# Optimization experiments

Hardware: AMD Instinct MI355X
Metric: run time of the kernel (lower is better)

## Reference

```python
import jax, jax.numpy as jnp
import numpy as np

B, N, QD = 1, 4096, 1024
H, DH = 16, 64  # heads, dim_head; inner_dim = H*DH = 1024
SCALE = DH ** -0.5


def setup_inputs() -> dict:
    key = jax.random.key(0)
    ks = jax.random.split(key, 6)
    inner = H * DH
    return {
        "x": jax.random.normal(ks[0], (B, N, QD), dtype=jnp.float32),
        "Wq": jax.random.normal(ks[1], (QD, inner), dtype=jnp.float32) * (QD ** -0.5),
        "Wk": jax.random.normal(ks[2], (QD, inner), dtype=jnp.float32) * (QD ** -0.5),
        "Wv": jax.random.normal(ks[3], (QD, inner), dtype=jnp.float32) * (QD ** -0.5),
        "Wo": jax.random.normal(ks[4], (inner, QD), dtype=jnp.float32) * (inner ** -0.5),
        "bo": jnp.zeros((QD,), dtype=jnp.float32),
    }


def reference(x, Wq, Wk, Wv, Wo, bo):
    b, n, _ = x.shape
    # projections, split heads: b n (h d) -> b h n d
    q = (x @ Wq).reshape(b, n, H, DH).transpose(0, 2, 1, 3)
    k = (x @ Wk).reshape(b, n, H, DH).transpose(0, 2, 1, 3)
    v = (x @ Wv).reshape(b, n, H, DH).transpose(0, 2, 1, 3)
    # fp32-forced QK^T (ATTN_PRECISION='fp32' path), then scale
    sim = jnp.einsum("bhid,bhjd->bhij", q.astype(jnp.float32), k.astype(jnp.float32)) * SCALE
    attn = jax.nn.softmax(sim, axis=-1)
    out = jnp.einsum("bhij,bhjd->bhid", attn, v)  # b h n d
    out = out.transpose(0, 2, 1, 3).reshape(b, n, H * DH)  # merge heads
    return out @ Wo + bo
```

## Files before the change

### kernel.cpp

```cpp
#include <hip/hip_runtime.h>
#include <stdint.h>

#define NH 16
#define NN 4096

typedef __attribute__((ext_vector_type(8))) short bf16x8;
typedef __attribute__((ext_vector_type(4))) short bf16x4;
typedef __attribute__((ext_vector_type(4))) float f32x4;
typedef __attribute__((ext_vector_type(16))) float f32x16;
typedef unsigned short u16;
typedef unsigned int u32;
typedef __attribute__((ext_vector_type(4))) u32 u32x4;

__device__ __forceinline__ u16 f2bf(float f) {
  u32 u = __float_as_uint(f);
  return (u16)((u + 0x7FFFu + ((u >> 16) & 1u)) >> 16);
}

#define GLD16(gp, lp)                                              \
  __builtin_amdgcn_global_load_lds(                                \
      (__attribute__((address_space(1))) void*)(gp),               \
      (__attribute__((address_space(3))) void*)(lp), 16, 0, 0)

__global__ __launch_bounds__(256) void cvt_bf16_kernel(const float* __restrict__ src,
                                                       u16* __restrict__ dst, int n) {
  int i = (blockIdx.x * blockDim.x + threadIdx.x) * 8;
  if (i >= n) return;
  float4 a = *(const float4*)(src + i);
  float4 b = *(const float4*)(src + i + 4);
  uint4 o;
  o.x = (u32)f2bf(a.x) | ((u32)f2bf(a.y) << 16);
  o.y = (u32)f2bf(a.z) | ((u32)f2bf(a.w) << 16);
  o.z = (u32)f2bf(b.x) | ((u32)f2bf(b.y) << 16);
  o.w = (u32)f2bf(b.z) | ((u32)f2bf(b.w) << 16);
  *(uint4*)(dst + i) = o;
}

__global__ __launch_bounds__(256) void transpose4(const float* __restrict__ Wq,
                                                  const float* __restrict__ Wk,
                                                  const float* __restrict__ Wv,
                                                  const float* __restrict__ Wo,
                                                  u16* __restrict__ Wqt, u16* __restrict__ Wkt,
                                                  u16* __restrict__ Wvt, u16* __restrict__ Wot) {
  __shared__ float tile[64][65];
  const float* src;
  u16* dst;
  float scale = 1.0f;
  int z = blockIdx.z;
  if (z == 0) { src = Wq; dst = Wqt; scale = 0.125f * 1.4426950408889634f; }
  else if (z == 1) { src = Wk; dst = Wkt; }
  else if (z == 2) { src = Wv; dst = Wvt; }
  else { src = Wo; dst = Wot; }
  int tx = threadIdx.x & 63, ty = threadIdx.x >> 6;
  int c0 = blockIdx.x * 64, r0 = blockIdx.y * 64;
#pragma unroll
  for (int i = ty; i < 64; i += 4)
    tile[i][tx] = src[(size_t)(r0 + i) * 1024 + c0 + tx];
  __syncthreads();
#pragma unroll
  for (int i = ty; i < 64; i += 4)
    dst[(size_t)(c0 + i) * 1024 + r0 + tx] = f2bf(tile[tx][i] * scale);
}

__global__ __launch_bounds__(256) void gemm_qkv(const u16* __restrict__ A,
                                                const u16* __restrict__ Bt,
                                                u16* __restrict__ Qb, u16* __restrict__ Kb,
                                                u16* __restrict__ Vth) {
  __shared__ __align__(16) u16 A_lds[2][128 * 32];
  __shared__ __align__(16) u16 B_lds[2][128 * 32];
  const int tid = threadIdx.x;
  const int l = tid & 63, w = tid >> 6;
  const int g = l >> 4, c = l & 15;
  const int wr = w >> 1, wc = w & 1;
  const int m0 = blockIdx.y * 128, n0 = blockIdx.x * 128;

  const int srow = tid >> 2;
  const u32 sswz = (u32)(((tid & 3) * 16) ^ ((srow & 3) << 4));
  const char* Ag = (const char*)A + (size_t)(m0 + srow) * 2048 + sswz;
  const char* Bg = (const char*)Bt + (size_t)(n0 + srow) * 2048 + sswz;
  const u32 ldsb = (u32)(w * 1024);

#define GSTAGE(buf, ks_)                                                          \
  do {                                                                            \
    u32 koff_ = (u32)(ks_) * 64;                                                  \
    _Pragma("unroll") for (int p_ = 0; p_ < 2; ++p_) {                            \
      GLD16(Ag + koff_ + (size_t)p_ * 64 * 2048,                                  \
            (char*)A_lds[buf] + p_ * 4096 + ldsb);                                \
      GLD16(Bg + koff_ + (size_t)p_ * 64 * 2048,                                  \
            (char*)B_lds[buf] + p_ * 4096 + ldsb);                                \
    }                                                                             \
  } while (0)

  f32x4 acc[4][4];
#pragma unroll
  for (int i = 0; i < 4; ++i)
#pragma unroll
    for (int j = 0; j < 4; ++j) acc[i][j] = (f32x4){0.f, 0.f, 0.f, 0.f};

  int cur = 0;
  GSTAGE(0, 0);
  for (int ks = 0; ks < 32; ++ks) {
    GSTAGE(cur ^ 1, (ks + 1) & 31);
    asm volatile("s_waitcnt vmcnt(4)" ::: "memory");
    __builtin_amdgcn_s_barrier();
    __builtin_amdgcn_sched_barrier(0);
    const char* Ac = (const char*)A_lds[cur];
    const char* Bc = (const char*)B_lds[cur];
    bf16x8 af[4], bfr[4];
#pragma unroll
    for (int i = 0; i < 4; ++i) {
      int row = wr * 64 + i * 16 + c;
      af[i] = *(const bf16x8*)(Ac + row * 64 + ((g * 16) ^ ((row & 3) << 4)));
    }
#pragma unroll
    for (int j = 0; j < 4; ++j) {
      int row = wc * 64 + j * 16 + c;
      bfr[j] = *(const bf16x8*)(Bc + row * 64 + ((g * 16) ^ ((row & 3) << 4)));
    }
    __builtin_amdgcn_s_setprio(1);
#pragma unroll
    for (int i = 0; i < 4; ++i)
#pragma unroll
      for (int j = 0; j < 4; ++j)
        acc[i][j] = __builtin_amdgcn_mfma_f32_16x16x32_bf16(af[i], bfr[j], acc[i][j], 0, 0, 0);
    __builtin_amdgcn_s_setprio(0);
    asm volatile("s_waitcnt lgkmcnt(0)" ::: "memory");
    __builtin_amdgcn_s_barrier();
    __builtin_amdgcn_sched_barrier(0);
    cur ^= 1;
  }
#undef GSTAGE

  const int sec = n0 >> 10;
  const int gq = ((g & 1) << 1) | (g >> 1);
#pragma unroll
  for (int i = 0; i < 4; ++i)
#pragma unroll
    for (int j = 0; j < 4; ++j)
#pragma unroll
      for (int r = 0; r < 4; ++r) {
        int m = m0 + wr * 64 + i * 16 + g * 4 + r;
        int col = n0 + wc * 64 + j * 16 + c;
        int cc = col & 1023;
        u16 v = f2bf(acc[i][j][r]);
        if (sec == 0) Qb[(size_t)m * 1024 + cc] = v;
        else if (sec == 1) Kb[(size_t)m * 1024 + cc] = v;
        else {
          int mq = m0 + wr * 64 + i * 16 + gq * 4 + r;
          Vth[(size_t)cc * 4096 + mq] = v;
        }
      }
}

__global__ __launch_bounds__(256) void gemm_out128(const u16* __restrict__ A,
                                                   const u16* __restrict__ Bt,
                                                   float* __restrict__ out,
                                                   const float* __restrict__ bias) {
  __shared__ __align__(16) u16 A_lds[2][128 * 32];
  __shared__ __align__(16) u16 B_lds[2][64 * 32];
  const int tid = threadIdx.x;
  const int l = tid & 63, w = tid >> 6;
  const int g = l >> 4, c = l & 15;
  const int m0 = blockIdx.y * 128, n0 = blockIdx.x * 64;

  const int srow = tid >> 2;
  const u32 sswz = (u32)(((tid & 3) * 16) ^ ((srow & 3) << 4));
  const char* Ag = (const char*)A + (size_t)(m0 + srow) * 2048 + sswz;
  const char* Bg = (const char*)Bt + (size_t)(n0 + srow) * 2048 + sswz;
  const u32 ldsb = (u32)(w * 1024);

#define GSTAGE3(buf, ks_)                                                         \
  do {                                                                            \
    u32 koff_ = (u32)(ks_) * 64;                                                  \
    GLD16(Ag + koff_, (char*)A_lds[buf] + ldsb);                                  \
    GLD16(Ag + koff_ + (size_t)64 * 2048, (char*)A_lds[buf] + 4096 + ldsb);       \
    GLD16(Bg + koff_, (char*)B_lds[buf] + ldsb);                                  \
  } while (0)

  f32x4 acc[2][4];
#pragma unroll
  for (int i = 0; i < 2; ++i)
#pragma unroll
    for (int j = 0; j < 4; ++j) acc[i][j] = (f32x4){0.f, 0.f, 0.f, 0.f};

  int cur = 0;
  GSTAGE3(0, 0);
  for (int ks = 0; ks < 32; ++ks) {
    GSTAGE3(cur ^ 1, (ks + 1) & 31);
    asm volatile("s_waitcnt vmcnt(3)" ::: "memory");
    __builtin_amdgcn_s_barrier();
    __builtin_amdgcn_sched_barrier(0);
    const char* Ac = (const char*)A_lds[cur];
    const char* Bc = (const char*)B_lds[cur];
    bf16x8 af[2], bfr[4];
#pragma unroll
    for (int i = 0; i < 2; ++i) {
      int row = w * 32 + i * 16 + c;
      af[i] = *(const bf16x8*)(Ac + row * 64 + ((g * 16) ^ ((row & 3) << 4)));
    }
#pragma unroll
    for (int j = 0; j < 4; ++j) {
      int row = j * 16 + c;
      bfr[j] = *(const bf16x8*)(Bc + row * 64 + ((g * 16) ^ ((row & 3) << 4)));
    }
    __builtin_amdgcn_s_setprio(1);
#pragma unroll
    for (int i = 0; i < 2; ++i)
#pragma unroll
      for (int j = 0; j < 4; ++j)
        acc[i][j] = __builtin_amdgcn_mfma_f32_16x16x32_bf16(af[i], bfr[j], acc[i][j], 0, 0, 0);
    __builtin_amdgcn_s_setprio(0);
    asm volatile("s_waitcnt lgkmcnt(0)" ::: "memory");
    __builtin_amdgcn_s_barrier();
    __builtin_amdgcn_sched_barrier(0);
    cur ^= 1;
  }
#undef GSTAGE3

#pragma unroll
  for (int i = 0; i < 2; ++i)
#pragma unroll
    for (int j = 0; j < 4; ++j)
#pragma unroll
      for (int r = 0; r < 4; ++r) {
        int m = m0 + w * 32 + i * 16 + g * 4 + r;
        int col = n0 + j * 16 + c;
        out[(size_t)m * 1024 + col] = acc[i][j][r] + bias[col];
      }
}

template <int SPLIT>
__global__ __launch_bounds__(256, 2) void flash_attn_t(const u16* __restrict__ Qb,
                                                       const u16* __restrict__ Kb,
                                                       const u16* __restrict__ Vt,
                                                       u16* __restrict__ Ob,
                                                       float* __restrict__ Op,
                                                       float* __restrict__ Lp) {
  constexpr int NT = SPLIT ? 32 : 64;
  __shared__ __align__(16) u16 K_lds[2][64 * 64];
  __shared__ __align__(16) u16 V_lds[2][64 * 64];
  const int tid = threadIdx.x;
  const int l = tid & 63, w = tid >> 6;
  const int lq = l & 31, hi = l >> 5;
  const int h = blockIdx.y;
  const int z = SPLIT ? blockIdx.z : 0;
  const int kb = z * 32;
  const int qb = blockIdx.x * 256 + w * 64;
  const int q0 = qb + lq, q1 = qb + 32 + lq;

  bf16x8 qf0[4], qf1[4];
  {
    const u16* qr0 = Qb + (size_t)q0 * 1024 + h * 64;
    const u16* qr1 = Qb + (size_t)q1 * 1024 + h * 64;
#pragma unroll
    for (int dm = 0; dm < 4; ++dm) {
      qf0[dm] = *(const bf16x8*)(qr0 + dm * 16 + hi * 8);
      qf1[dm] = *(const bf16x8*)(qr1 + dm * 16 + hi * 8);
    }
  }

  f32x16 ot0[2], ot1[2];
#pragma unroll
  for (int a = 0; a < 2; ++a)
#pragma unroll
    for (int r = 0; r < 16; ++r) { ot0[a][r] = 0.f; ot1[a][r] = 0.f; }
  float lrow0 = 0.f, lrow1 = 0.f;
  u32 pkA0[16], pkA1[16], pkB0[16], pkB1[16];

  const int srow = tid >> 3;
  const u32 sswz = (u32)(((tid & 7) * 16) ^ ((srow & 7) << 4));
  const char* Kg = (const char*)Kb + ((size_t)srow * 1024 + h * 64) * 2 + sswz;
  const char* Vg = (const char*)Vt + ((size_t)(h * 64 + srow) * 4096) * 2 + sswz;
  const u32 ldsb = (u32)(w * 1024);

#define PVONLY(P0, P1, VSLOT)                                                     \
  {                                                                               \
    const char* Vp_ = (const char*)(VSLOT);                                       \
    __builtin_amdgcn_s_setprio(1);                                                \
    _Pragma("unroll") for (int sti_ = 0; sti_ < 4; ++sti_) {                      \
      u32x4 pw0_ = {P0[sti_ * 4 + 0], P0[sti_ * 4 + 1], P0[sti_ * 4 + 2],         \
                    P0[sti_ * 4 + 3]};                                            \
      u32x4 pw1_ = {P1[sti_ * 4 + 0], P1[sti_ * 4 + 1], P1[sti_ * 4 + 2],         \
                    P1[sti_ * 4 + 3]};                                            \
      bf16x8 pf0_ = __builtin_bit_cast(bf16x8, pw0_);                             \
      bf16x8 pf1_ = __builtin_bit_cast(bf16x8, pw1_);                             \
      const u32 cb_ = (u32)(sti_ * 32 + hi * 16);                                 \
      _Pragma("unroll") for (int a_ = 0; a_ < 2; ++a_) {                          \
        const int rowd_ = a_ * 32 + lq;                                           \
        const u32 rs_ = (u32)(rowd_ * 128), rz_ = (u32)((rowd_ & 7) << 4);        \
        bf16x8 vf_ = *(const bf16x8*)(Vp_ + rs_ + (cb_ ^ rz_));                   \
        ot0[a_] = __builtin_amdgcn_mfma_f32_32x32x16_bf16(vf_, pf0_, ot0[a_], 0, 0, 0); \
        ot1[a_] = __builtin_amdgcn_mfma_f32_32x32x16_bf16(vf_, pf1_, ot1[a_], 0, 0, 0); \
      }                                                                           \
    }                                                                             \
    __builtin_amdgcn_s_setprio(0);                                                \
  }

#define BODY(TI, C0, C1, P0, P1, DOPREV)                                          \
  {                                                                               \
    const int ti_ = (TI);                                                         \
    const int nxt_ = (ti_ + 1) & (NT - 1);                                        \
    {                                                                             \
      const char* kg_ = Kg + (size_t)(kb + nxt_) * 64 * 2048;                     \
      char* kl_ = (char*)K_lds[nxt_ & 1] + ldsb;                                  \
      GLD16(kg_, kl_);                                                            \
      GLD16(kg_ + 32 * 2048, kl_ + 4096);                                         \
      const char* vg_ = Vg + (size_t)(kb + ti_) * 128;                            \
      char* vl_ = (char*)V_lds[ti_ & 1] + ldsb;                                   \
      GLD16(vg_, vl_);                                                            \
      GLD16(vg_ + (size_t)32 * 8192, vl_ + 4096);                                 \
    }                                                                             \
    asm volatile("s_waitcnt vmcnt(4)" ::: "memory");                              \
    __builtin_amdgcn_s_barrier();                                                 \
    __builtin_amdgcn_sched_barrier(0);                                            \
    const char* Kc_ = (const char*)K_lds[ti_ & 1];                                \
    f32x16 st0_[2], st1_[2];                                                      \
    _Pragma("unroll") for (int s_ = 0; s_ < 2; ++s_)                              \
    _Pragma("unroll") for (int r_ = 0; r_ < 16; ++r_) {                           \
      st0_[s_][r_] = 0.f;                                                         \
      st1_[s_][r_] = 0.f;                                                         \
    }                                                                             \
    __builtin_amdgcn_s_setprio(1);                                                \
    _Pragma("unroll") for (int s_ = 0; s_ < 2; ++s_) {                            \
      const int row_ = s_ * 32 + lq;                                              \
      const u32 rs_ = (u32)(row_ * 128), rz_ = (u32)((row_ & 7) << 4);            \
      _Pragma("unroll") for (int dm_ = 0; dm_ < 4; ++dm_) {                       \
        bf16x8 kf_ = *(const bf16x8*)(Kc_ + rs_ + ((u32)(dm_ * 32 + hi * 16) ^ rz_)); \
        st0_[s_] = __builtin_amdgcn_mfma_f32_32x32x16_bf16(kf_, qf0[dm_], st0_[s_], 0, 0, 0); \
        st1_[s_] = __builtin_amdgcn_mfma_f32_32x32x16_bf16(kf_, qf1[dm_], st1_[s_], 0, 0, 0); \
      }                                                                           \
    }                                                                             \
    __builtin_amdgcn_s_setprio(0);                                                \
    if (DOPREV) PVONLY(P0, P1, V_lds[(ti_ - 1) & 1]);                             \
    float rs0_ = 0.f, rs1_ = 0.f;                                                 \
    _Pragma("unroll") for (int s_ = 0; s_ < 2; ++s_)                              \
    _Pragma("unroll") for (int j_ = 0; j_ < 8; ++j_) {                            \
      float a0_ = __builtin_amdgcn_exp2f(st0_[s_][2 * j_]);                       \
      float a1_ = __builtin_amdgcn_exp2f(st0_[s_][2 * j_ + 1]);                   \
      rs0_ += a0_ + a1_;                                                          \
      u32 wp0_;                                                                   \
      asm("v_cvt_pk_bf16_f32 %0, %1, %2" : "=v"(wp0_) : "v"(a0_), "v"(a1_));      \
      C0[s_ * 8 + j_] = wp0_;                                                     \
      float b0_ = __builtin_amdgcn_exp2f(st1_[s_][2 * j_]);                       \
      float b1_ = __builtin_amdgcn_exp2f(st1_[s_][2 * j_ + 1]);                   \
      rs1_ += b0_ + b1_;                                                          \
      u32 wp1_;                                                                   \
      asm("v_cvt_pk_bf16_f32 %0, %1, %2" : "=v"(wp1_) : "v"(b0_), "v"(b1_));      \
      C1[s_ * 8 + j_] = wp1_;                                                     \
    }                                                                             \
    lrow0 += rs0_;                                                                \
    lrow1 += rs1_;                                                                \
    asm volatile("s_waitcnt lgkmcnt(0)" ::: "memory");                            \
    __builtin_amdgcn_s_barrier();                                                 \
    __builtin_amdgcn_sched_barrier(0);                                            \
  }

  {
    const char* kg0 = Kg + (size_t)kb * 64 * 2048;
    char* kl = (char*)K_lds[0] + ldsb;
    GLD16(kg0, kl);
    GLD16(kg0 + 32 * 2048, kl + 4096);
  }

  BODY(0, pkA0, pkA1, pkA0, pkA1, 0);
  for (int i = 1; i < NT - 1; i += 2) {
    BODY(i, pkB0, pkB1, pkA0, pkA1, 1);
    BODY(i + 1, pkA0, pkA1, pkB0, pkB1, 1);
  }
  BODY(NT - 1, pkB0, pkB1, pkA0, pkA1, 1);
  asm volatile("s_waitcnt vmcnt(0)" ::: "memory");
  __builtin_amdgcn_s_barrier();
  __builtin_amdgcn_sched_barrier(0);
  PVONLY(pkB0, pkB1, V_lds[(NT - 1) & 1]);

#undef BODY
#undef PVONLY

  lrow0 += __shfl_xor(lrow0, 32, 64);
  lrow1 += __shfl_xor(lrow1, 32, 64);
  if constexpr (SPLIT) {
    float* or0 = Op + (size_t)z * (4096 * 1024) + (size_t)q0 * 1024 + h * 64 + hi * 4;
    float* or1 = Op + (size_t)z * (4096 * 1024) + (size_t)q1 * 1024 + h * 64 + hi * 4;
#pragma unroll
    for (int a = 0; a < 2; ++a)
#pragma unroll
      for (int rr = 0; rr < 4; ++rr) {
        float4 f0 = {ot0[a][rr * 4 + 0], ot0[a][rr * 4 + 1], ot0[a][rr * 4 + 2],
                     ot0[a][rr * 4 + 3]};
        *(float4*)(or0 + a * 32 + rr * 8) = f0;
        float4 f1 = {ot1[a][rr * 4 + 0], ot1[a][rr * 4 + 1], ot1[a][rr * 4 + 2],
                     ot1[a][rr * 4 + 3]};
        *(float4*)(or1 + a * 32 + rr * 8) = f1;
      }
    if (hi == 0) {
      Lp[z * 65536 + h * 4096 + q0] = lrow0;
      Lp[z * 65536 + h * 4096 + q1] = lrow1;
    }
  } else {
    float inv0 = 1.f / lrow0, inv1 = 1.f / lrow1;
    u16* or0 = Ob + (size_t)q0 * 1024 + h * 64 + hi * 4;
    u16* or1 = Ob + (size_t)q1 * 1024 + h * 64 + hi * 4;
#pragma unroll
    for (int a = 0; a < 2; ++a)
#pragma unroll
      for (int rr = 0; rr < 4; ++rr) {
        ushort4 o4;
        o4.x = f2bf(ot0[a][rr * 4 + 0] * inv0);
        o4.y = f2bf(ot0[a][rr * 4 + 1] * inv0);
        o4.z = f2bf(ot0[a][rr * 4 + 2] * inv0);
        o4.w = f2bf(ot0[a][rr * 4 + 3] * inv0);
        *(ushort4*)(or0 + a * 32 + rr * 8) = o4;
        o4.x = f2bf(ot1[a][rr * 4 + 0] * inv1);
        o4.y = f2bf(ot1[a][rr * 4 + 1] * inv1);
        o4.z = f2bf(ot1[a][rr * 4 + 2] * inv1);
        o4.w = f2bf(ot1[a][rr * 4 + 3] * inv1);
        *(ushort4*)(or1 + a * 32 + rr * 8) = o4;
      }
  }
}

__global__ __launch_bounds__(256) void merge_halves(const float* __restrict__ O0,
                                                    const float* __restrict__ O1,
                                                    const float* __restrict__ L0,
                                                    const float* __restrict__ L1,
                                                    u16* __restrict__ Ob) {
  int idx = blockIdx.x * 256 + threadIdx.x;
  int q = idx >> 7;
  int c0 = (idx & 127) * 8;
  int h = c0 >> 6;
  float inv = 1.f / (L0[h * 4096 + q] + L1[h * 4096 + q]);
  size_t off = (size_t)q * 1024 + c0;
  float4 a0 = *(const float4*)(O0 + off), a1 = *(const float4*)(O0 + off + 4);
  float4 b0 = *(const float4*)(O1 + off), b1 = *(const float4*)(O1 + off + 4);
  ushort4 o0, o1;
  o0.x = f2bf((a0.x + b0.x) * inv);
  o0.y = f2bf((a0.y + b0.y) * inv);
  o0.z = f2bf((a0.z + b0.z) * inv);
  o0.w = f2bf((a0.w + b0.w) * inv);
  o1.x = f2bf((a1.x + b1.x) * inv);
  o1.y = f2bf((a1.y + b1.y) * inv);
  o1.z = f2bf((a1.z + b1.z) * inv);
  o1.w = f2bf((a1.w + b1.w) * inv);
  *(ushort4*)(Ob + off) = o0;
  *(ushort4*)(Ob + off + 4) = o1;
}

extern "C" void kernel_launch(void* const* d_in, const int* in_sizes, int n_in,
                              void* d_out, int out_size, void* d_ws, size_t ws_size,
                              hipStream_t stream) {
  const float* x = (const float*)d_in[0];
  const float* Wq = (const float*)d_in[1];
  const float* Wk = (const float*)d_in[2];
  const float* Wv = (const float*)d_in[3];
  const float* Wo = (const float*)d_in[4];
  const float* bo = (const float*)d_in[5];
  float* out = (float*)d_out;

  char* ws = (char*)d_ws;
  u16* xb  = (u16*)(ws);
  u16* Wqt = (u16*)(ws + (8u << 20));
  u16* Wot = (u16*)(ws + (14u << 20));
  u16* Qb  = (u16*)(ws + (16u << 20));
  u16* Kbf = (u16*)(ws + (24u << 20));
  u16* Vth = (u16*)(ws + (32u << 20));
  u16* Ob  = (u16*)(ws + (40u << 20));
  float* Op = (float*)(ws + (40u << 20));
  float* Lp = (float*)(ws + (72u << 20));
  u16* Wkt = Wqt + (1u << 20);
  u16* Wvt = Wqt + (2u << 20);

  const bool split = ws_size >= ((73u << 20) + (1u << 19));

  cvt_bf16_kernel<<<2048, 256, 0, stream>>>(x, xb, 4096 * 1024);
  transpose4<<<dim3(16, 16, 4), 256, 0, stream>>>(Wq, Wk, Wv, Wo, Wqt, Wkt, Wvt, Wot);
  gemm_qkv<<<dim3(24, 32), 256, 0, stream>>>(xb, Wqt, Qb, Kbf, Vth);

  if (split) {
    flash_attn_t<1><<<dim3(16, 16, 2), 256, 0, stream>>>(Qb, Kbf, Vth, nullptr, Op, Lp);
    u16* ObM = (u16*)ws;
    merge_halves<<<2048, 256, 0, stream>>>(Op, Op + (1u << 22), Lp, Lp + 65536, ObM);
    gemm_out128<<<dim3(16, 32), 256, 0, stream>>>(ObM, Wot, out, bo);
  } else {
    flash_attn_t<0><<<dim3(16, 16, 1), 256, 0, stream>>>(Qb, Kbf, Vth, Ob, nullptr, nullptr);
    gemm_out128<<<dim3(16, 32), 256, 0, stream>>>(Ob, Wot, out, bo);
  }
}
```

Baseline: 188.9 us.

## Merge prep kernels, coalesce V-transpose stores via LDS, deepen attention pipeline

Merges the x-to-bf16 conversion and the weight transposes into one launch to save a kernel launch. The QKV GEMM epilogue now stages the transposed V tile through a swizzled LDS buffer so it can issue 16-byte coalesced global stores instead of scattered 2-byte writes. The flash-attention loop uses four K/V LDS slots and processes two KV tiles per barrier pair, interleaving QK, softmax and PV across tiles to halve barriers and prefetch further ahead. This doubles attention LDS use, which may reduce occupancy.

```diff
diff --git a/kernel.cpp b/kernel.cpp
--- a/kernel.cpp
+++ b/kernel.cpp
@@ -22,36 +22,42 @@
       (__attribute__((address_space(1))) void*)(gp),               \
       (__attribute__((address_space(3))) void*)(lp), 16, 0, 0)
 
-__global__ __launch_bounds__(256) void cvt_bf16_kernel(const float* __restrict__ src,
-                                                       u16* __restrict__ dst, int n) {
-  int i = (blockIdx.x * blockDim.x + threadIdx.x) * 8;
-  if (i >= n) return;
-  float4 a = *(const float4*)(src + i);
-  float4 b = *(const float4*)(src + i + 4);
-  uint4 o;
-  o.x = (u32)f2bf(a.x) | ((u32)f2bf(a.y) << 16);
-  o.y = (u32)f2bf(a.z) | ((u32)f2bf(a.w) << 16);
-  o.z = (u32)f2bf(b.x) | ((u32)f2bf(b.y) << 16);
-  o.w = (u32)f2bf(b.z) | ((u32)f2bf(b.w) << 16);
-  *(uint4*)(dst + i) = o;
-}
-
-__global__ __launch_bounds__(256) void transpose4(const float* __restrict__ Wq,
-                                                  const float* __restrict__ Wk,
-                                                  const float* __restrict__ Wv,
-                                                  const float* __restrict__ Wo,
-                                                  u16* __restrict__ Wqt, u16* __restrict__ Wkt,
-                                                  u16* __restrict__ Wvt, u16* __restrict__ Wot) {
+__global__ __launch_bounds__(256) void prep(const float* __restrict__ x,
+                                            const float* __restrict__ Wq,
+                                            const float* __restrict__ Wk,
+                                            const float* __restrict__ Wv,
+                                            const float* __restrict__ Wo,
+                                            u16* __restrict__ xb,
+                                            u16* __restrict__ Wqt, u16* __restrict__ Wkt,
+                                            u16* __restrict__ Wvt, u16* __restrict__ Wot) {
   __shared__ float tile[64][65];
+  int z = blockIdx.z;
+  int tid = threadIdx.x;
+  if (z >= 4) {
+    int bi = (z - 4) * 256 + blockIdx.y * 16 + blockIdx.x;
+    size_t base = (size_t)bi * 8192;
+#pragma unroll
+    for (int k = 0; k < 4; ++k) {
+      size_t i = base + (size_t)k * 2048 + tid * 8;
+      float4 a = *(const float4*)(x + i);
+      float4 b = *(const float4*)(x + i + 4);
+      uint4 o;
+      o.x = (u32)f2bf(a.x) | ((u32)f2bf(a.y) << 16);
+      o.y = (u32)f2bf(a.z) | ((u32)f2bf(a.w) << 16);
+      o.z = (u32)f2bf(b.x) | ((u32)f2bf(b.y) << 16);
+      o.w = (u32)f2bf(b.z) | ((u32)f2bf(b.w) << 16);
+      *(uint4*)(xb + i) = o;
+    }
+    return;
+  }
   const float* src;
   u16* dst;
   float scale = 1.0f;
-  int z = blockIdx.z;
   if (z == 0) { src = Wq; dst = Wqt; scale = 0.125f * 1.4426950408889634f; }
   else if (z == 1) { src = Wk; dst = Wkt; }
   else if (z == 2) { src = Wv; dst = Wvt; }
   else { src = Wo; dst = Wot; }
-  int tx = threadIdx.x & 63, ty = threadIdx.x >> 6;
+  int tx = tid & 63, ty = tid >> 6;
   int c0 = blockIdx.x * 64, r0 = blockIdx.y * 64;
 #pragma unroll
   for (int i = ty; i < 64; i += 4)
@@ -66,8 +72,9 @@
                                                 const u16* __restrict__ Bt,
                                                 u16* __restrict__ Qb, u16* __restrict__ Kb,
                                                 u16* __restrict__ Vth) {
-  __shared__ __align__(16) u16 A_lds[2][128 * 32];
-  __shared__ __align__(16) u16 B_lds[2][128 * 32];
+  __shared__ __align__(16) u16 SH[16384];
+  u16* A_lds = SH;
+  u16* B_lds = SH + 8192;
   const int tid = threadIdx.x;
   const int l = tid & 63, w = tid >> 6;
   const int g = l >> 4, c = l & 15;
@@ -85,9 +92,9 @@
     u32 koff_ = (u32)(ks_) * 64;                                                  \
     _Pragma("unroll") for (int p_ = 0; p_ < 2; ++p_) {                            \
       GLD16(Ag + koff_ + (size_t)p_ * 64 * 2048,                                  \
-            (char*)A_lds[buf] + p_ * 4096 + ldsb);                                \
+            (char*)A_lds + (buf) * 8192 + p_ * 4096 + ldsb);                      \
       GLD16(Bg + koff_ + (size_t)p_ * 64 * 2048,                                  \
-            (char*)B_lds[buf] + p_ * 4096 + ldsb);                                \
+            (char*)B_lds + (buf) * 8192 + p_ * 4096 + ldsb);                      \
     }                                                                             \
   } while (0)
 
@@ -104,8 +111,8 @@
     asm volatile("s_waitcnt vmcnt(4)" ::: "memory");
     __builtin_amdgcn_s_barrier();
     __builtin_amdgcn_sched_barrier(0);
-    const char* Ac = (const char*)A_lds[cur];
-    const char* Bc = (const char*)B_lds[cur];
+    const char* Ac = (const char*)A_lds + cur * 8192;
+    const char* Bc = (const char*)B_lds + cur * 8192;
     bf16x8 af[4], bfr[4];
 #pragma unroll
     for (int i = 0; i < 4; ++i) {
@@ -132,24 +139,44 @@
 #undef GSTAGE
 
   const int sec = n0 >> 10;
-  const int gq = ((g & 1) << 1) | (g >> 1);
-#pragma unroll
-  for (int i = 0; i < 4; ++i)
-#pragma unroll
-    for (int j = 0; j < 4; ++j)
-#pragma unroll
-      for (int r = 0; r < 4; ++r) {
-        int m = m0 + wr * 64 + i * 16 + g * 4 + r;
-        int col = n0 + wc * 64 + j * 16 + c;
-        int cc = col & 1023;
-        u16 v = f2bf(acc[i][j][r]);
-        if (sec == 0) Qb[(size_t)m * 1024 + cc] = v;
-        else if (sec == 1) Kb[(size_t)m * 1024 + cc] = v;
-        else {
-          int mq = m0 + wr * 64 + i * 16 + gq * 4 + r;
-          Vth[(size_t)cc * 4096 + mq] = v;
+  if (sec < 2) {
+#pragma unroll
+    for (int i = 0; i < 4; ++i)
+#pragma unroll
+      for (int j = 0; j < 4; ++j)
+#pragma unroll
+        for (int r = 0; r < 4; ++r) {
+          int m = m0 + wr * 64 + i * 16 + g * 4 + r;
+          int cc = (n0 + wc * 64 + j * 16 + c) & 1023;
+          u16 v = f2bf(acc[i][j][r]);
+          if (sec == 0) Qb[(size_t)m * 1024 + cc] = v;
+          else Kb[(size_t)m * 1024 + cc] = v;
         }
+  } else {
+    const int gq = ((g & 1) << 1) | (g >> 1);
+    const int cc0 = n0 & 1023;
+#pragma unroll
+    for (int i = 0; i < 4; ++i)
+#pragma unroll
+      for (int j = 0; j < 4; ++j)
+#pragma unroll
+        for (int r = 0; r < 4; ++r) {
+          int cl = wc * 64 + j * 16 + c;
+          int mql = wr * 64 + i * 16 + gq * 4 + r;
+          SH[cl * 128 + (mql ^ ((cl & 15) << 3))] = f2bf(acc[i][j][r]);
+        }
+    __syncthreads();
+#pragma unroll
+    for (int p = 0; p < 4; ++p) {
+      int row = p * 32 + (tid >> 3);
+#pragma unroll
+      for (int half = 0; half < 2; ++half) {
+        int mq = (tid & 7) * 8 + half * 64;
+        bf16x8 vv = *(const bf16x8*)&SH[row * 128 + (mq ^ ((row & 15) << 3))];
+        *(bf16x8*)(Vth + (size_t)(cc0 + row) * 4096 + m0 + mq) = vv;
       }
+    }
+  }
 }
 
 __global__ __launch_bounds__(256) void gemm_out128(const u16* __restrict__ A,
@@ -237,8 +264,9 @@
                                                        float* __restrict__ Op,
                                                        float* __restrict__ Lp) {
   constexpr int NT = SPLIT ? 32 : 64;
-  __shared__ __align__(16) u16 K_lds[2][64 * 64];
-  __shared__ __align__(16) u16 V_lds[2][64 * 64];
+  constexpr int NB = NT / 2;
+  __shared__ __align__(16) u16 K_lds[4][64 * 64];
+  __shared__ __align__(16) u16 V_lds[4][64 * 64];
   const int tid = threadIdx.x;
   const int l = tid & 63, w = tid >> 6;
   const int lq = l & 31, hi = l >> 5;
@@ -265,7 +293,7 @@
 #pragma unroll
     for (int r = 0; r < 16; ++r) { ot0[a][r] = 0.f; ot1[a][r] = 0.f; }
   float lrow0 = 0.f, lrow1 = 0.f;
-  u32 pkA0[16], pkA1[16], pkB0[16], pkB1[16];
+  u32 pkP0[16], pkP1[16], pkX0[16], pkX1[16];
 
   const int srow = tid >> 3;
   const u32 sswz = (u32)(((tid & 7) * 16) ^ ((srow & 7) << 4));
@@ -273,9 +301,67 @@
   const char* Vg = (const char*)Vt + ((size_t)(h * 64 + srow) * 4096) * 2 + sswz;
   const u32 ldsb = (u32)(w * 1024);
 
-#define PVONLY(P0, P1, VSLOT)                                                     \
+#define STAGE_K(T, SLOT)                                                          \
   {                                                                               \
-    const char* Vp_ = (const char*)(VSLOT);                                       \
+    const char* kg_ = Kg + (size_t)(kb + ((T) & (NT - 1))) * 64 * 2048;           \
+    char* kl_ = (char*)K_lds[SLOT] + ldsb;                                        \
+    GLD16(kg_, kl_);                                                              \
+    GLD16(kg_ + 32 * 2048, kl_ + 4096);                                           \
+  }
+#define STAGE_V(T, SLOT)                                                          \
+  {                                                                               \
+    const char* vg_ = Vg + (size_t)(kb + ((T) & (NT - 1))) * 128;                 \
+    char* vl_ = (char*)V_lds[SLOT] + ldsb;                                        \
+    GLD16(vg_, vl_);                                                              \
+    GLD16(vg_ + (size_t)32 * 8192, vl_ + 4096);                                   \
+  }
+
+#define QK2(SLOT, ST0, ST1)                                                       \
+  {                                                                               \
+    const char* Kc_ = (const char*)K_lds[SLOT];                                   \
+    _Pragma("unroll") for (int s_ = 0; s_ < 2; ++s_)                              \
+    _Pragma("unroll") for (int r_ = 0; r_ < 16; ++r_) {                           \
+      ST0[s_][r_] = 0.f;                                                          \
+      ST1[s_][r_] = 0.f;                                                          \
+    }                                                                             \
+    __builtin_amdgcn_s_setprio(1);                                                \
+    _Pragma("unroll") for (int s_ = 0; s_ < 2; ++s_) {                            \
+      const int row_ = s_ * 32 + lq;                                              \
+      const u32 rs_ = (u32)(row_ * 128), rz_ = (u32)((row_ & 7) << 4);            \
+      _Pragma("unroll") for (int dm_ = 0; dm_ < 4; ++dm_) {                       \
+        bf16x8 kf_ = *(const bf16x8*)(Kc_ + rs_ + ((u32)(dm_ * 32 + hi * 16) ^ rz_)); \
+        ST0[s_] = __builtin_amdgcn_mfma_f32_32x32x16_bf16(kf_, qf0[dm_], ST0[s_], 0, 0, 0); \
+        ST1[s_] = __builtin_amdgcn_mfma_f32_32x32x16_bf16(kf_, qf1[dm_], ST1[s_], 0, 0, 0); \
+      }                                                                           \
+    }                                                                             \
+    __builtin_amdgcn_s_setprio(0);                                                \
+  }
+
+#define SM2(ST0, ST1, D0, D1)                                                     \
+  {                                                                               \
+    float rs0_ = 0.f, rs1_ = 0.f;                                                 \
+    _Pragma("unroll") for (int s_ = 0; s_ < 2; ++s_)                              \
+    _Pragma("unroll") for (int j_ = 0; j_ < 8; ++j_) {                            \
+      float a0_ = __builtin_amdgcn_exp2f(ST0[s_][2 * j_]);                        \
+      float a1_ = __builtin_amdgcn_exp2f(ST0[s_][2 * j_ + 1]);                    \
+      rs0_ += a0_ + a1_;                                                          \
+      u32 wp0_;                                                                   \
+      asm("v_cvt_pk_bf16_f32 %0, %1, %2" : "=v"(wp0_) : "v"(a0_), "v"(a1_));      \
+      D0[s_ * 8 + j_] = wp0_;                                                     \
+      float b0_ = __builtin_amdgcn_exp2f(ST1[s_][2 * j_]);                        \
+      float b1_ = __builtin_amdgcn_exp2f(ST1[s_][2 * j_ + 1]);                    \
+      rs1_ += b0_ + b1_;                                                          \
+      u32 wp1_;                                                                   \
+      asm("v_cvt_pk_bf16_f32 %0, %1, %2" : "=v"(wp1_) : "v"(b0_), "v"(b1_));      \
+      D1[s_ * 8 + j_] = wp1_;                                                     \
+    }                                                                             \
+    lrow0 += rs0_;                                                                \
+    lrow1 += rs1_;                                                                \
+  }
+
+#define PV2(P0, P1, SLOT)                                                         \
+  {                                                                               \
+    const char* Vp_ = (const char*)V_lds[SLOT];                                   \
     __builtin_amdgcn_s_setprio(1);                                                \
     _Pragma("unroll") for (int sti_ = 0; sti_ < 4; ++sti_) {                      \
       u32x4 pw0_ = {P0[sti_ * 4 + 0], P0[sti_ * 4 + 1], P0[sti_ * 4 + 2],         \
@@ -296,85 +382,48 @@
     __builtin_amdgcn_s_setprio(0);                                                \
   }
 
-#define BODY(TI, C0, C1, P0, P1, DOPREV)                                          \
+#define BODY2(T0, SK0r, SK1r, SKs0, SKs1, SVp, SV0r, SVs0, SVs1, DOPREV)          \
   {                                                                               \
-    const int ti_ = (TI);                                                         \
-    const int nxt_ = (ti_ + 1) & (NT - 1);                                        \
-    {                                                                             \
-      const char* kg_ = Kg + (size_t)(kb + nxt_) * 64 * 2048;                     \
-      char* kl_ = (char*)K_lds[nxt_ & 1] + ldsb;                                  \
-      GLD16(kg_, kl_);                                                            \
-      GLD16(kg_ + 32 * 2048, kl_ + 4096);                                         \
-      const char* vg_ = Vg + (size_t)(kb + ti_) * 128;                            \
-      char* vl_ = (char*)V_lds[ti_ & 1] + ldsb;                                   \
-      GLD16(vg_, vl_);                                                            \
-      GLD16(vg_ + (size_t)32 * 8192, vl_ + 4096);                                 \
-    }                                                                             \
-    asm volatile("s_waitcnt vmcnt(4)" ::: "memory");                              \
+    STAGE_K((T0) + 2, SKs0);                                                      \
+    STAGE_K((T0) + 3, SKs1);                                                      \
+    STAGE_V((T0) + 1, SVs0);                                                      \
+    STAGE_V((T0) + 2, SVs1);                                                      \
+    asm volatile("s_waitcnt vmcnt(8)" ::: "memory");                              \
     __builtin_amdgcn_s_barrier();                                                 \
     __builtin_amdgcn_sched_barrier(0);                                            \
-    const char* Kc_ = (const char*)K_lds[ti_ & 1];                                \
     f32x16 st0_[2], st1_[2];                                                      \
-    _Pragma("unroll") for (int s_ = 0; s_ < 2; ++s_)                              \
-    _Pragma("unroll") for (int r_ = 0; r_ < 16; ++r_) {                           \
-      st0_[s_][r_] = 0.f;                                                         \
-      st1_[s_][r_] = 0.f;                                                         \
-    }                                                                             \
-    __builtin_amdgcn_s_setprio(1);                                                \
-    _Pragma("unroll") for (int s_ = 0; s_ < 2; ++s_) {                            \
-      const int row_ = s_ * 32 + lq;                                              \
-      const u32 rs_ = (u32)(row_ * 128), rz_ = (u32)((row_ & 7) << 4);            \
-      _Pragma("unroll") for (int dm_ = 0; dm_ < 4; ++dm_) {                       \
-        bf16x8 kf_ = *(const bf16x8*)(Kc_ + rs_ + ((u32)(dm_ * 32 + hi * 16) ^ rz_)); \
-        st0_[s_] = __builtin_amdgcn_mfma_f32_32x32x16_bf16(kf_, qf0[dm_], st0_[s_], 0, 0, 0); \
-        st1_[s_] = __builtin_amdgcn_mfma_f32_32x32x16_bf16(kf_, qf1[dm_], st1_[s_], 0, 0, 0); \
-      }                                                                           \
-    }                                                                             \
-    __builtin_amdgcn_s_setprio(0);                                                \
-    if (DOPREV) PVONLY(P0, P1, V_lds[(ti_ - 1) & 1]);                             \
-    float rs0_ = 0.f, rs1_ = 0.f;                                                 \
-    _Pragma("unroll") for (int s_ = 0; s_ < 2; ++s_)                              \
-    _Pragma("unroll") for (int j_ = 0; j_ < 8; ++j_) {                            \
-      float a0_ = __builtin_amdgcn_exp2f(st0_[s_][2 * j_]);                       \
-      float a1_ = __builtin_amdgcn_exp2f(st0_[s_][2 * j_ + 1]);                   \
-      rs0_ += a0_ + a1_;                                                          \
-      u32 wp0_;                                                                   \
-      asm("v_cvt_pk_bf16_f32 %0, %1, %2" : "=v"(wp0_) : "v"(a0_), "v"(a1_));      \
-      C0[s_ * 8 + j_] = wp0_;                                                     \
-      float b0_ = __builtin_amdgcn_exp2f(st1_[s_][2 * j_]);                       \
-      float b1_ = __builtin_amdgcn_exp2f(st1_[s_][2 * j_ + 1]);                   \
-      rs1_ += b0_ + b1_;                                                          \
-      u32 wp1_;                                                                   \
-      asm("v_cvt_pk_bf16_f32 %0, %1, %2" : "=v"(wp1_) : "v"(b0_), "v"(b1_));      \
-      C1[s_ * 8 + j_] = wp1_;                                                     \
-    }                                                                             \
-    lrow0 += rs0_;                                                                \
-    lrow1 += rs1_;                                                                \
+    QK2(SK0r, st0_, st1_);                                                        \
+    SM2(st0_, st1_, pkX0, pkX1);                                                  \
+    if (DOPREV) PV2(pkP0, pkP1, SVp);                                             \
+    QK2(SK1r, st0_, st1_);                                                        \
+    PV2(pkX0, pkX1, SV0r);                                                        \
+    SM2(st0_, st1_, pkP0, pkP1);                                                  \
     asm volatile("s_waitcnt lgkmcnt(0)" ::: "memory");                            \
     __builtin_amdgcn_s_barrier();                                                 \
     __builtin_amdgcn_sched_barrier(0);                                            \
   }
 
-  {
-    const char* kg0 = Kg + (size_t)kb * 64 * 2048;
-    char* kl = (char*)K_lds[0] + ldsb;
-    GLD16(kg0, kl);
-    GLD16(kg0 + 32 * 2048, kl + 4096);
-  }
-
-  BODY(0, pkA0, pkA1, pkA0, pkA1, 0);
-  for (int i = 1; i < NT - 1; i += 2) {
-    BODY(i, pkB0, pkB1, pkA0, pkA1, 1);
-    BODY(i + 1, pkA0, pkA1, pkB0, pkB1, 1);
-  }
-  BODY(NT - 1, pkB0, pkB1, pkA0, pkA1, 1);
-  asm volatile("s_waitcnt vmcnt(0)" ::: "memory");
+  STAGE_K(0, 0);
+  STAGE_K(1, 1);
+  STAGE_V(0, 0);
+
+  BODY2(0, 0, 1, 2, 3, 3, 0, 1, 2, 0);
+  for (int b = 1; b + 1 < NB; b += 2) {
+    BODY2(2 * b, 2, 3, 0, 1, 1, 2, 3, 0, 1);
+    BODY2(2 * (b + 1), 0, 1, 2, 3, 3, 0, 1, 2, 1);
+  }
+  BODY2(2 * (NB - 1), 2, 3, 0, 1, 1, 2, 3, 0, 1);
+  asm volatile("s_waitcnt vmcnt(0) lgkmcnt(0)" ::: "memory");
   __builtin_amdgcn_s_barrier();
   __builtin_amdgcn_sched_barrier(0);
-  PVONLY(pkB0, pkB1, V_lds[(NT - 1) & 1]);
-
-#undef BODY
-#undef PVONLY
+  PV2(pkP0, pkP1, 3);
+
+#undef BODY2
+#undef PV2
+#undef SM2
+#undef QK2
+#undef STAGE_K
+#undef STAGE_V
 
   lrow0 += __shfl_xor(lrow0, 32, 64);
   lrow1 += __shfl_xor(lrow1, 32, 64);
@@ -471,8 +520,7 @@
 
   const bool split = ws_size >= ((73u << 20) + (1u << 19));
 
-  cvt_bf16_kernel<<<2048, 256, 0, stream>>>(x, xb, 4096 * 1024);
-  transpose4<<<dim3(16, 16, 4), 256, 0, stream>>>(Wq, Wk, Wv, Wo, Wqt, Wkt, Wvt, Wot);
+  prep<<<dim3(16, 16, 6), 256, 0, stream>>>(x, Wq, Wk, Wv, Wo, xb, Wqt, Wkt, Wvt, Wot);
   gemm_qkv<<<dim3(24, 32), 256, 0, stream>>>(xb, Wqt, Qb, Kbf, Vth);
 
   if (split) {
```

New measurement: 174.3 us. -7.7%, faster.
